# Optimization experiments

Measured on AMD Instinct MI355X. Metric: run time of the kernel, lower is better.

Reference implementation:

```python
import jax, jax.numpy as jnp
import numpy as np

B, S, D, H = 2, 2048, 1024, 16
DK = D // H


def setup_inputs() -> dict:
    key = jax.random.key(0)
    ks = jax.random.split(key, 11)
    scale = jnp.float32(1.0 / np.sqrt(D))
    inp = {
        "query": jax.random.normal(ks[0], (B, S, D), jnp.float32),
        "key": jax.random.normal(ks[1], (B, S, D), jnp.float32),
        "value": jax.random.normal(ks[2], (B, S, D), jnp.float32),
        # causal mask: True = masked (masked_fill semantics), broadcast over batch/heads
        "mask": jnp.triu(jnp.ones((S, S), dtype=bool), k=1)[None, None, :, :],
        "Wq": jax.random.normal(ks[3], (D, D), jnp.float32) * scale,
        "bq": jnp.zeros((D,), jnp.float32),
        "Wk": jax.random.normal(ks[4], (D, D), jnp.float32) * scale,
        "bk": jnp.zeros((D,), jnp.float32),
        "Wv": jax.random.normal(ks[5], (D, D), jnp.float32) * scale,
        "bv": jnp.zeros((D,), jnp.float32),
        "Wo": jax.random.normal(ks[6], (D, D), jnp.float32) * scale,
        "bo": jnp.zeros((D,), jnp.float32),
    }
    return inp


def _split_heads(x):
    # (B, S, D) -> (B, H, S, DK)
    b, s, _ = x.shape
    return x.reshape(b, s, H, DK).transpose(0, 2, 1, 3)


def reference(query, key, value, mask, Wq, bq, Wk, bk, Wv, bv, Wo, bo):
    # nn.Linear: y = x @ W.T + b
    q = _split_heads(query @ Wq.T + bq)
    k = _split_heads(key @ Wk.T + bk)
    v = _split_heads(value @ Wv.T + bv)

    inv_sqrt_dk = jnp.float32(1.0 / np.sqrt(DK))
    scores = jnp.einsum("bhqd,bhkd->bhqk", q, k) * inv_sqrt_dk  # (B,H,S,S)
    scores = jnp.where(mask, jnp.float32(-jnp.inf), scores)
    weights = jax.nn.softmax(scores, axis=-1)
    weights = jnp.nan_to_num(weights, nan=0.0)  # fully-masked rows -> 0

    attn = jnp.einsum("bhqk,bhkd->bhqd", weights, v)  # (B,H,S,DK)
    merged = attn.transpose(0, 2, 1, 3).reshape(B, S, D)  # merge heads
    return merged @ Wo.T + bo
```

## Files before the change

### kernel.cpp

```cpp
#include <hip/hip_runtime.h>


typedef unsigned short u16;
typedef unsigned int u32;
typedef __attribute__((ext_vector_type(8))) __bf16 bf16x8;
typedef __attribute__((ext_vector_type(8))) unsigned short us8;
typedef __attribute__((ext_vector_type(4))) float f32x4;

#define S_LEN 2048
#define D_DIM 1024
#define NH 16
#define DKH 64
#define Mi 1048576ULL

__device__ __forceinline__ u16 f2bf(float f) {
  return __builtin_bit_cast(u16, (__bf16)f);
}
__device__ __forceinline__ bf16x8 ld_frag(const u16* p) {
  us8 v = *(const us8*)p;
  return __builtin_bit_cast(bf16x8, v);
}
__device__ __forceinline__ void gl2lds16(const u16* g, u16* l) {
  __builtin_amdgcn_global_load_lds(
      (__attribute__((address_space(1))) void*)(g),
      (__attribute__((address_space(3))) void*)(l), 16, 0, 0);
}

__global__ __launch_bounds__(256, 1) void cvt_all(
    const float* __restrict__ q, const float* __restrict__ k, const float* __restrict__ v,
    const float* __restrict__ wq, const float* __restrict__ wk,
    const float* __restrict__ wv, const float* __restrict__ wo,
    u16* __restrict__ dst)
{
  size_t e0 = ((size_t)blockIdx.x * 256 + threadIdx.x) * 8;
  const float* s;
  if      (e0 <  4*Mi) s = q  + e0;
  else if (e0 <  8*Mi) s = k  + (e0 - 4*Mi);
  else if (e0 < 12*Mi) s = v  + (e0 - 8*Mi);
  else if (e0 < 13*Mi) s = wq + (e0 - 12*Mi);
  else if (e0 < 14*Mi) s = wk + (e0 - 13*Mi);
  else if (e0 < 15*Mi) s = wv + (e0 - 14*Mi);
  else                 s = wo + (e0 - 15*Mi);
  float4 a = ((const float4*)s)[0];
  float4 b = ((const float4*)s)[1];
  us8 o;
  o[0]=f2bf(a.x); o[1]=f2bf(a.y); o[2]=f2bf(a.z); o[3]=f2bf(a.w);
  o[4]=f2bf(b.x); o[5]=f2bf(b.y); o[6]=f2bf(b.z); o[7]=f2bf(b.w);
  *(us8*)(dst + e0) = o;
}

__global__ __launch_bounds__(256, 1) void gemm_qkv_bb(
    const u16* __restrict__ Aq, const u16* __restrict__ Ak, const u16* __restrict__ Av,
    const u16* __restrict__ Wqb, const u16* __restrict__ Wkb, const u16* __restrict__ Wvb,
    const float* __restrict__ bq, const float* __restrict__ bk, const float* __restrict__ bv,
    u16* __restrict__ Oq, u16* __restrict__ Ok, u16* __restrict__ Ov, float qscale)
{
  const int z = blockIdx.z;
  const u16* A = (z == 0) ? Aq : (z == 1) ? Ak : Av;
  const u16* W = (z == 0) ? Wqb : (z == 1) ? Wkb : Wvb;
  const float* bias = (z == 0) ? bq : (z == 1) ? bk : bv;
  u16* out = (z == 0) ? Oq : (z == 1) ? Ok : Ov;
  const float scale = (z == 0) ? qscale : 1.0f;
  const int K = 1024;

  __shared__ u16 lA[128 * 32];
  __shared__ u16 lB[128 * 32];
  const int t = threadIdx.x;
  const int w = t >> 6, l = t & 63;
  const int mblk = blockIdx.y * 128, nblk = blockIdx.x * 128;
  const int wm = (w & 1) * 64, wn = (w >> 1) * 64;
  const int lr = l & 15, lq = l >> 4;
  const int srow = l >> 2, scol = (l & 3) * 8;

  f32x4 acc[4][4] = {};

  for (int k0 = 0; k0 < K; k0 += 32) {
    __syncthreads();
    #pragma unroll
    for (int r = 0; r < 2; ++r) {
      int grp = r * 4 + w;
      gl2lds16(A + (size_t)(mblk + grp * 16 + srow) * K + k0 + scol, &lA[grp * 512]);
      gl2lds16(W + (size_t)(nblk + grp * 16 + srow) * K + k0 + scol, &lB[grp * 512]);
    }
    __syncthreads();
    bf16x8 aF[4], bF[4];
    #pragma unroll
    for (int mt = 0; mt < 4; ++mt)
      aF[mt] = ld_frag(&lA[(wm + mt * 16 + lr) * 32 + lq * 8]);
    #pragma unroll
    for (int nt = 0; nt < 4; ++nt)
      bF[nt] = ld_frag(&lB[(wn + nt * 16 + lr) * 32 + lq * 8]);
    #pragma unroll
    for (int mt = 0; mt < 4; ++mt)
      #pragma unroll
      for (int nt = 0; nt < 4; ++nt)
        acc[mt][nt] = __builtin_amdgcn_mfma_f32_16x16x32_bf16(aF[mt], bF[nt], acc[mt][nt], 0, 0, 0);
  }

  #pragma unroll
  for (int mt = 0; mt < 4; ++mt)
    #pragma unroll
    for (int nt = 0; nt < 4; ++nt)
      #pragma unroll
      for (int r = 0; r < 4; ++r) {
        int rowg = mblk + wm + mt * 16 + lq * 4 + r;
        int colg = nblk + wn + nt * 16 + lr;
        float v = (acc[mt][nt][r] + bias[colg]) * scale;
        int b = rowg >> 11, s = rowg & 2047;
        int h = colg >> 6, dk = colg & 63;
        if (z != 2)
          out[(((size_t)(b * NH + h)) * S_LEN + s) * DKH + dk] = f2bf(v);
        else
          out[(((size_t)(b * NH + h)) * DKH + dk) * S_LEN + s] = f2bf(v);
      }
}

__global__ __launch_bounds__(256, 1) void gemm_out_bb(
    const u16* __restrict__ A, const u16* __restrict__ W,
    const float* __restrict__ bias, float* __restrict__ out)
{
  const int K = 1024;
  __shared__ u16 lA[128 * 32];
  __shared__ u16 lB[64 * 32];
  const int t = threadIdx.x;
  const int w = t >> 6, l = t & 63;
  const int mblk = blockIdx.y * 128, nblk = blockIdx.x * 64;
  const int wm = (w & 1) * 64, wn = (w >> 1) * 32;
  const int lr = l & 15, lq = l >> 4;
  const int srow = l >> 2, scol = (l & 3) * 8;

  f32x4 acc[4][2] = {};

  for (int k0 = 0; k0 < K; k0 += 32) {
    __syncthreads();
    #pragma unroll
    for (int r = 0; r < 2; ++r) {
      int grp = r * 4 + w;
      gl2lds16(A + (size_t)(mblk + grp * 16 + srow) * K + k0 + scol, &lA[grp * 512]);
    }
    gl2lds16(W + (size_t)(nblk + w * 16 + srow) * K + k0 + scol, &lB[w * 512]);
    __syncthreads();
    bf16x8 aF[4], bF[2];
    #pragma unroll
    for (int mt = 0; mt < 4; ++mt)
      aF[mt] = ld_frag(&lA[(wm + mt * 16 + lr) * 32 + lq * 8]);
    #pragma unroll
    for (int nt = 0; nt < 2; ++nt)
      bF[nt] = ld_frag(&lB[(wn + nt * 16 + lr) * 32 + lq * 8]);
    #pragma unroll
    for (int mt = 0; mt < 4; ++mt)
      #pragma unroll
      for (int nt = 0; nt < 2; ++nt)
        acc[mt][nt] = __builtin_amdgcn_mfma_f32_16x16x32_bf16(aF[mt], bF[nt], acc[mt][nt], 0, 0, 0);
  }

  #pragma unroll
  for (int mt = 0; mt < 4; ++mt)
    #pragma unroll
    for (int nt = 0; nt < 2; ++nt)
      #pragma unroll
      for (int r = 0; r < 4; ++r) {
        int rowg = mblk + wm + mt * 16 + lq * 4 + r;
        int colg = nblk + wn + nt * 16 + lr;
        out[(size_t)rowg * D_DIM + colg] = acc[mt][nt][r] + bias[colg];
      }
}

__global__ __launch_bounds__(256, 1) void attn_fused(
    const u16* __restrict__ Q, const u16* __restrict__ K,
    const u16* __restrict__ Vt, u16* __restrict__ O)
{
  __shared__ u16 lK[2][64 * 64];
  __shared__ u16 lV[2][64 * 64];

  const int idx = blockIdx.x;
  const int s_ = idx >> 8;
  const int r_ = idx & 255;
  const int bh = r_ & 31;
  const int t_ = r_ >> 5;
  const int qt = (s_ == 0) ? t_ : (s_ == 1) ? 31 - t_ : (s_ == 2) ? 8 + t_ : 23 - t_;
  const int b = bh >> 4, h = bh & 15;
  const int t = threadIdx.x;
  const int w = t >> 6, l = t & 63;
  const int lr = l & 15, lq = l >> 4;

  const u16* Qp = Q + (size_t)bh * S_LEN * DKH;
  const u16* Kp = K + (size_t)bh * S_LEN * DKH;
  const u16* Vp = Vt + (size_t)bh * DKH * S_LEN;

  const int srow8 = l >> 3;
  const int schunk = l & 7;

  const int qrow = qt * 64 + w * 16 + lr;
  bf16x8 qf[2];
  qf[0] = ld_frag(Qp + (size_t)qrow * DKH + lq * 8);
  qf[1] = ld_frag(Qp + (size_t)qrow * DKH + 32 + lq * 8);

  f32x4 o[4] = {};
  f32x4 li4 = {};

  #pragma unroll
  for (int r2 = 0; r2 < 2; ++r2) {
    int grp = r2 * 4 + w;
    int row = grp * 8 + srow8;
    int sw = (row & 3) | (((row >> 3) & 1) << 2);
    int c = schunk ^ sw;
    gl2lds16(Kp + (size_t)row * DKH + c * 8, &lK[0][grp * 512]);
    gl2lds16(Vp + (size_t)row * S_LEN + c * 8, &lV[0][grp * 512]);
  }

  for (int kt = 0; kt <= qt; ++kt) {
    const int cur = kt & 1;
    __syncthreads();

    if (kt < qt) {
      #pragma unroll
      for (int r2 = 0; r2 < 2; ++r2) {
        int grp = r2 * 4 + w;
        int row = grp * 8 + srow8;
        int sw = (row & 3) | (((row >> 3) & 1) << 2);
        int c = schunk ^ sw;
        gl2lds16(Kp + (size_t)((kt + 1) * 64 + row) * DKH + c * 8, &lK[cur ^ 1][grp * 512]);
        gl2lds16(Vp + (size_t)row * S_LEN + (kt + 1) * 64 + c * 8, &lV[cur ^ 1][grp * 512]);
      }
    }

    f32x4 st[4] = {};
    #pragma unroll
    for (int ksd = 0; ksd < 2; ++ksd)
      #pragma unroll
      for (int nt = 0; nt < 4; ++nt) {
        int sig = 32 * (nt >> 1) + 8 * (lr >> 2) + 4 * (nt & 1) + (lr & 3);
        int slot = (ksd * 4 + lq) ^ (lr & 7);
        bf16x8 kb = ld_frag(&lK[cur][sig * 64 + slot * 8]);
        st[nt] = __builtin_amdgcn_mfma_f32_16x16x32_bf16(kb, qf[ksd], st[nt], 0, 0, 0);
      }

    float p[4][4];
    const bool diag = (kt == qt);
    const int qloc = w * 16 + lr;
    #pragma unroll
    for (int nt = 0; nt < 4; ++nt)
      #pragma unroll
      for (int r = 0; r < 4; ++r) {
        int kk = 32 * (nt >> 1) + 8 * lq + 4 * (nt & 1) + r;
        float e = exp2f(st[nt][r]);
        p[nt][r] = (diag && kk > qloc) ? 0.0f : e;
        li4[r] += p[nt][r];
      }

    #pragma unroll
    for (int ks = 0; ks < 2; ++ks) {
      us8 av;
      #pragma unroll
      for (int j = 0; j < 4; ++j) {
        av[j] = f2bf(p[2 * ks][j]);
        av[4 + j] = f2bf(p[2 * ks + 1][j]);
      }
      bf16x8 pa = __builtin_bit_cast(bf16x8, av);
      #pragma unroll
      for (int dblk = 0; dblk < 4; ++dblk) {
        int d = dblk * 16 + lr;
        int sw = (d & 3) | (((d >> 3) & 1) << 2);
        int slot = (4 * ks + lq) ^ sw;
        bf16x8 vb = ld_frag(&lV[cur][d * 64 + slot * 8]);
        o[dblk] = __builtin_amdgcn_mfma_f32_16x16x32_bf16(pa, vb, o[dblk], 0, 0, 0);
      }
    }
  }

  float li = li4[0] + li4[1] + li4[2] + li4[3];
  li += __shfl_xor(li, 16);
  li += __shfl_xor(li, 32);
  float ri[4];
  #pragma unroll
  for (int r = 0; r < 4; ++r) ri[r] = 1.0f / __shfl(li, lq * 4 + r);

  const size_t obase = ((size_t)b * S_LEN + qt * 64 + w * 16) * D_DIM + h * DKH;
  #pragma unroll
  for (int dblk = 0; dblk < 4; ++dblk)
    #pragma unroll
    for (int r = 0; r < 4; ++r)
      O[obase + (size_t)(lq * 4 + r) * D_DIM + dblk * 16 + lr] = f2bf(o[dblk][r] * ri[r]);
}

extern "C" void kernel_launch(void* const* d_in, const int* in_sizes, int n_in,
                              void* d_out, int out_size, void* d_ws, size_t ws_size,
                              hipStream_t stream) {
  const float* query = (const float*)d_in[0];
  const float* key   = (const float*)d_in[1];
  const float* value = (const float*)d_in[2];
  const float* Wq = (const float*)d_in[4];
  const float* bq = (const float*)d_in[5];
  const float* Wk = (const float*)d_in[6];
  const float* bk = (const float*)d_in[7];
  const float* Wv = (const float*)d_in[8];
  const float* bv = (const float*)d_in[9];
  const float* Wo = (const float*)d_in[10];
  const float* bo = (const float*)d_in[11];
  float* out = (float*)d_out;

  const float qscale = 0.125f * 1.44269504088896341f;
  dim3 blk(256);

  u16* base = (u16*)d_ws;
  u16* Qb = base;
  u16* Kb = base + 4 * Mi;
  u16* Vb = base + 8 * Mi;

  u16* cvt = base + 12 * Mi;
  u16* qbf = cvt;
  u16* kbf = cvt + 4 * Mi;
  u16* vbf = cvt + 8 * Mi;
  u16* wqb = cvt + 12 * Mi;
  u16* wkb = cvt + 13 * Mi;
  u16* wvb = cvt + 14 * Mi;
  u16* wob = cvt + 15 * Mi;
  u16* Ab  = qbf;

  cvt_all<<<dim3(8192), blk, 0, stream>>>(query, key, value, Wq, Wk, Wv, Wo, cvt);
  gemm_qkv_bb<<<dim3(8, 32, 3), blk, 0, stream>>>(qbf, kbf, vbf, wqb, wkb, wvb,
                                                  bq, bk, bv, Qb, Kb, Vb, qscale);
  attn_fused<<<dim3(1024), blk, 0, stream>>>(Qb, Kb, Vb, Ab);
  gemm_out_bb<<<dim3(16, 32), blk, 0, stream>>>(Ab, wob, bo, out);
}
```

Measured before the change: 233.4 us.

## Rewrite QKV projection GEMM as 256x256 8-wave ping-pong pipelined kernel

Replaces the 128x128 single-buffered QKV GEMM with a 256x256-tile, 512-thread kernel. It double-buffers LDS with global_load_lds prefetch, XOR-swizzles the LDS layout to avoid bank conflicts, interleaves the MFMA quadrants with fragment loads under s_setprio, and remaps block IDs across XCDs. The aim is to hide global-load latency and raise MFMA utilisation. In exchange it uses 128 KB of LDS and only 192 blocks, and the hand-placed waitcnt and barrier ordering is fragile.

Result: slower. 249.1 us (+6.7%).

```diff
diff --git a/kernel.cpp b/kernel.cpp
--- a/kernel.cpp
+++ b/kernel.cpp
@@ -49,63 +49,150 @@
   *(us8*)(dst + e0) = o;
 }
 
-__global__ __launch_bounds__(256, 1) void gemm_qkv_bb(
+__device__ __forceinline__ void stage_op(const u16* __restrict__ g, int rowbase, int k0,
+                                         u16* h0, u16* h1, int w, int srow, int scol) {
+  #pragma unroll
+  for (int hh = 0; hh < 2; ++hh) {
+    u16* dst = hh ? h1 : h0;
+    #pragma unroll
+    for (int i = 0; i < 2; ++i) {
+      int rr = hh * 128 + w * 16 + i * 8 + srow;
+      gl2lds16(g + (size_t)(rowbase + rr) * 1024 + k0 + scol, dst + (w * 2 + i) * 512);
+    }
+  }
+}
+
+__global__ __launch_bounds__(512, 2) void gemm_qkv_8p(
     const u16* __restrict__ Aq, const u16* __restrict__ Ak, const u16* __restrict__ Av,
     const u16* __restrict__ Wqb, const u16* __restrict__ Wkb, const u16* __restrict__ Wvb,
     const float* __restrict__ bq, const float* __restrict__ bk, const float* __restrict__ bv,
     u16* __restrict__ Oq, u16* __restrict__ Ok, u16* __restrict__ Ov, float qscale)
 {
-  const int z = blockIdx.z;
+  __shared__ u16 lds[2][4][8192];
+
+  const int o  = ((int)blockIdx.x & 7) * 24 + ((int)blockIdx.x >> 3);
+  const int z  = o >> 6;
+  const int r_ = o & 63;
+  const int mblk = (r_ >> 2) * 256;
+  const int nblk = (r_ & 3) * 256;
+
   const u16* A = (z == 0) ? Aq : (z == 1) ? Ak : Av;
   const u16* W = (z == 0) ? Wqb : (z == 1) ? Wkb : Wvb;
   const float* bias = (z == 0) ? bq : (z == 1) ? bk : bv;
   u16* out = (z == 0) ? Oq : (z == 1) ? Ok : Ov;
   const float scale = (z == 0) ? qscale : 1.0f;
-  const int K = 1024;
-
-  __shared__ u16 lA[128 * 32];
-  __shared__ u16 lB[128 * 32];
+
   const int t = threadIdx.x;
   const int w = t >> 6, l = t & 63;
-  const int mblk = blockIdx.y * 128, nblk = blockIdx.x * 128;
-  const int wm = (w & 1) * 64, wn = (w >> 1) * 64;
+  const int wr = w >> 2, wc = w & 3;
   const int lr = l & 15, lq = l >> 4;
-  const int srow = l >> 2, scol = (l & 3) * 8;
-
-  f32x4 acc[4][4] = {};
-
-  for (int k0 = 0; k0 < K; k0 += 32) {
-    __syncthreads();
-    #pragma unroll
-    for (int r = 0; r < 2; ++r) {
-      int grp = r * 4 + w;
-      gl2lds16(A + (size_t)(mblk + grp * 16 + srow) * K + k0 + scol, &lA[grp * 512]);
-      gl2lds16(W + (size_t)(nblk + grp * 16 + srow) * K + k0 + scol, &lB[grp * 512]);
-    }
-    __syncthreads();
-    bf16x8 aF[4], bF[4];
-    #pragma unroll
-    for (int mt = 0; mt < 4; ++mt)
-      aF[mt] = ld_frag(&lA[(wm + mt * 16 + lr) * 32 + lq * 8]);
+  const int srow = l >> 3;
+  const int scol = ((l & 7) ^ ((l >> 5) << 1)) * 8;
+  const int rb0 = (wc & 1) * 64;
+
+  #define IDX(r, kk) ((((r) * 64) + (kk) * 32 + lq * 8) ^ ((((r) >> 2) & 1) << 4))
+
+  f32x4 acc[8][4] = {};
+
+  stage_op(A, mblk, 0,  lds[0][0], lds[0][1], w, srow, scol);
+  stage_op(W, nblk, 0,  lds[0][2], lds[0][3], w, srow, scol);
+  stage_op(A, mblk, 64, lds[1][0], lds[1][1], w, srow, scol);
+  asm volatile("s_waitcnt vmcnt(4)" ::: "memory");
+  __builtin_amdgcn_s_barrier();
+
+  for (int kt = 0; kt < 16; ++kt) {
+    u16* lA = lds[kt & 1][wr];
+    u16* lB = lds[kt & 1][2 + (wc >> 1)];
+    u16 (*cur)[8192] = lds[kt & 1];
+    u16 (*nxt)[8192] = lds[(kt & 1) ^ 1];
+
+    bf16x8 aF[4][2], bF[4][2];
+
+    #pragma unroll
+    for (int am = 0; am < 4; ++am)
+      #pragma unroll
+      for (int kk = 0; kk < 2; ++kk)
+        aF[am][kk] = ld_frag(&lA[IDX(am * 16 + lr, kk)]);
+    #pragma unroll
+    for (int bn = 0; bn < 2; ++bn)
+      #pragma unroll
+      for (int kk = 0; kk < 2; ++kk)
+        bF[bn][kk] = ld_frag(&lB[IDX(rb0 + bn * 16 + lr, kk)]);
+    if (kt + 1 < 16) stage_op(W, nblk, (kt + 1) * 64, nxt[2], nxt[3], w, srow, scol);
+    __builtin_amdgcn_s_barrier();
+    asm volatile("s_waitcnt lgkmcnt(0)" ::: "memory");
+    __builtin_amdgcn_s_setprio(1);
+    #pragma unroll
+    for (int am = 0; am < 4; ++am)
+      #pragma unroll
+      for (int bn = 0; bn < 2; ++bn)
+        #pragma unroll
+        for (int kk = 0; kk < 2; ++kk)
+          acc[am][bn] = __builtin_amdgcn_mfma_f32_16x16x32_bf16(aF[am][kk], bF[bn][kk], acc[am][bn], 0, 0, 0);
+    __builtin_amdgcn_s_setprio(0);
+    __builtin_amdgcn_s_barrier();
+
+    #pragma unroll
+    for (int bn = 0; bn < 2; ++bn)
+      #pragma unroll
+      for (int kk = 0; kk < 2; ++kk)
+        bF[2 + bn][kk] = ld_frag(&lB[IDX(rb0 + 32 + bn * 16 + lr, kk)]);
+    __builtin_amdgcn_s_barrier();
+    asm volatile("s_waitcnt lgkmcnt(0)" ::: "memory");
+    __builtin_amdgcn_s_setprio(1);
+    #pragma unroll
+    for (int am = 0; am < 4; ++am)
+      #pragma unroll
+      for (int bn = 0; bn < 2; ++bn)
+        #pragma unroll
+        for (int kk = 0; kk < 2; ++kk)
+          acc[am][2 + bn] = __builtin_amdgcn_mfma_f32_16x16x32_bf16(aF[am][kk], bF[2 + bn][kk], acc[am][2 + bn], 0, 0, 0);
+    __builtin_amdgcn_s_setprio(0);
+    __builtin_amdgcn_s_barrier();
+
+    #pragma unroll
+    for (int am = 0; am < 4; ++am)
+      #pragma unroll
+      for (int kk = 0; kk < 2; ++kk)
+        aF[am][kk] = ld_frag(&lA[IDX(64 + am * 16 + lr, kk)]);
+    __builtin_amdgcn_s_barrier();
+    asm volatile("s_waitcnt lgkmcnt(0)" ::: "memory");
+    __builtin_amdgcn_s_setprio(1);
+    #pragma unroll
+    for (int am = 0; am < 4; ++am)
+      #pragma unroll
+      for (int bn = 0; bn < 2; ++bn)
+        #pragma unroll
+        for (int kk = 0; kk < 2; ++kk)
+          acc[4 + am][2 + bn] = __builtin_amdgcn_mfma_f32_16x16x32_bf16(aF[am][kk], bF[2 + bn][kk], acc[4 + am][2 + bn], 0, 0, 0);
+    __builtin_amdgcn_s_setprio(0);
+    __builtin_amdgcn_s_barrier();
+
+    if (kt + 2 < 16) stage_op(A, mblk, (kt + 2) * 64, cur[0], cur[1], w, srow, scol);
+    __builtin_amdgcn_s_setprio(1);
+    #pragma unroll
+    for (int am = 0; am < 4; ++am)
+      #pragma unroll
+      for (int bn = 0; bn < 2; ++bn)
+        #pragma unroll
+        for (int kk = 0; kk < 2; ++kk)
+          acc[4 + am][bn] = __builtin_amdgcn_mfma_f32_16x16x32_bf16(aF[am][kk], bF[bn][kk], acc[4 + am][bn], 0, 0, 0);
+    __builtin_amdgcn_s_setprio(0);
+    if (kt < 14)       asm volatile("s_waitcnt vmcnt(4)" ::: "memory");
+    else if (kt == 14) asm volatile("s_waitcnt vmcnt(0)" ::: "memory");
+    if (kt < 15) __builtin_amdgcn_s_barrier();
+  }
+  #undef IDX
+
+  #pragma unroll
+  for (int mt = 0; mt < 8; ++mt)
     #pragma unroll
     for (int nt = 0; nt < 4; ++nt)
-      bF[nt] = ld_frag(&lB[(wn + nt * 16 + lr) * 32 + lq * 8]);
-    #pragma unroll
-    for (int mt = 0; mt < 4; ++mt)
-      #pragma unroll
-      for (int nt = 0; nt < 4; ++nt)
-        acc[mt][nt] = __builtin_amdgcn_mfma_f32_16x16x32_bf16(aF[mt], bF[nt], acc[mt][nt], 0, 0, 0);
-  }
-
-  #pragma unroll
-  for (int mt = 0; mt < 4; ++mt)
-    #pragma unroll
-    for (int nt = 0; nt < 4; ++nt)
-      #pragma unroll
-      for (int r = 0; r < 4; ++r) {
-        int rowg = mblk + wm + mt * 16 + lq * 4 + r;
-        int colg = nblk + wn + nt * 16 + lr;
-        float v = (acc[mt][nt][r] + bias[colg]) * scale;
+      #pragma unroll
+      for (int rg = 0; rg < 4; ++rg) {
+        int rowg = mblk + wr * 128 + mt * 16 + lq * 4 + rg;
+        int colg = nblk + wc * 64 + nt * 16 + lr;
+        float v = (acc[mt][nt][rg] + bias[colg]) * scale;
         int b = rowg >> 11, s = rowg & 2047;
         int h = colg >> 6, dk = colg & 63;
         if (z != 2)
@@ -319,8 +406,8 @@
   u16* Ab  = qbf;
 
   cvt_all<<<dim3(8192), blk, 0, stream>>>(query, key, value, Wq, Wk, Wv, Wo, cvt);
-  gemm_qkv_bb<<<dim3(8, 32, 3), blk, 0, stream>>>(qbf, kbf, vbf, wqb, wkb, wvb,
-                                                  bq, bk, bv, Qb, Kb, Vb, qscale);
+  gemm_qkv_8p<<<dim3(192), dim3(512), 0, stream>>>(qbf, kbf, vbf, wqb, wkb, wvb,
+                                                   bq, bk, bv, Qb, Kb, Vb, qscale);
   attn_fused<<<dim3(1024), blk, 0, stream>>>(Qb, Kb, Vb, Ab);
   gemm_out_bb<<<dim3(16, 32), blk, 0, stream>>>(Ab, wob, bo, out);
 }
```

## Double-buffer LDS, swizzle LDS layout, and remap QKV GEMM blocks across XCDs

Applied to the files above, without the earlier changes.

Both bf16 GEMM kernels now use two LDS buffers. Each iteration prefetches the next K-slice while the current one feeds the MFMAs, which removes one barrier per iteration and overlaps global loads with compute. LDS columns are XOR-swizzled by row on both the store and the fragment-read side to reduce bank conflicts. The QKV GEMM moves to a 1D grid with a block-index remap that groups tiles per XCD for better L2 reuse. The cost is twice the shared memory and a dependence on async LDS loads completing at the single barrier.

After: 245.2 us. 5.1% more time.

```diff
diff --git a/kernel.cpp b/kernel.cpp
--- a/kernel.cpp
+++ b/kernel.cpp
@@ -55,7 +55,13 @@
     const float* __restrict__ bq, const float* __restrict__ bk, const float* __restrict__ bv,
     u16* __restrict__ Oq, u16* __restrict__ Ok, u16* __restrict__ Ov, float qscale)
 {
-  const int z = blockIdx.z;
+  const int bid = blockIdx.x;
+  const int o   = (bid & 7) * 96 + (bid >> 3);
+  const int z   = o >> 8;
+  const int rem = o & 255;
+  const int mblk = (rem >> 3) * 128;
+  const int nblk = (rem & 7) * 128;
+
   const u16* A = (z == 0) ? Aq : (z == 1) ? Ak : Av;
   const u16* W = (z == 0) ? Wqb : (z == 1) ? Wkb : Wvb;
   const float* bias = (z == 0) ? bq : (z == 1) ? bk : bv;
@@ -63,33 +69,43 @@
   const float scale = (z == 0) ? qscale : 1.0f;
   const int K = 1024;
 
-  __shared__ u16 lA[128 * 32];
-  __shared__ u16 lB[128 * 32];
+  __shared__ u16 lA[2][128 * 32];
+  __shared__ u16 lB[2][128 * 32];
   const int t = threadIdx.x;
   const int w = t >> 6, l = t & 63;
-  const int mblk = blockIdx.y * 128, nblk = blockIdx.x * 128;
   const int wm = (w & 1) * 64, wn = (w >> 1) * 64;
   const int lr = l & 15, lq = l >> 4;
-  const int srow = l >> 2, scol = (l & 3) * 8;
+  const int srow = l >> 2;
+  const int scol = ((l & 3) ^ ((l >> 3) & 3)) * 8;
+  const int rsw  = (lr >> 1) & 3;
 
   f32x4 acc[4][4] = {};
 
+  #pragma unroll
+  for (int r = 0; r < 2; ++r) {
+    int grp = r * 4 + w;
+    gl2lds16(A + (size_t)(mblk + grp * 16 + srow) * K + scol, &lA[0][grp * 512]);
+    gl2lds16(W + (size_t)(nblk + grp * 16 + srow) * K + scol, &lB[0][grp * 512]);
+  }
+
   for (int k0 = 0; k0 < K; k0 += 32) {
+    const int cur = (k0 >> 5) & 1;
     __syncthreads();
-    #pragma unroll
-    for (int r = 0; r < 2; ++r) {
-      int grp = r * 4 + w;
-      gl2lds16(A + (size_t)(mblk + grp * 16 + srow) * K + k0 + scol, &lA[grp * 512]);
-      gl2lds16(W + (size_t)(nblk + grp * 16 + srow) * K + k0 + scol, &lB[grp * 512]);
+    if (k0 + 32 < K) {
+      #pragma unroll
+      for (int r = 0; r < 2; ++r) {
+        int grp = r * 4 + w;
+        gl2lds16(A + (size_t)(mblk + grp * 16 + srow) * K + k0 + 32 + scol, &lA[cur ^ 1][grp * 512]);
+        gl2lds16(W + (size_t)(nblk + grp * 16 + srow) * K + k0 + 32 + scol, &lB[cur ^ 1][grp * 512]);
+      }
     }
-    __syncthreads();
     bf16x8 aF[4], bF[4];
     #pragma unroll
     for (int mt = 0; mt < 4; ++mt)
-      aF[mt] = ld_frag(&lA[(wm + mt * 16 + lr) * 32 + lq * 8]);
+      aF[mt] = ld_frag(&lA[cur][(wm + mt * 16 + lr) * 32 + (lq ^ rsw) * 8]);
     #pragma unroll
     for (int nt = 0; nt < 4; ++nt)
-      bF[nt] = ld_frag(&lB[(wn + nt * 16 + lr) * 32 + lq * 8]);
+      bF[nt] = ld_frag(&lB[cur][(wn + nt * 16 + lr) * 32 + (lq ^ rsw) * 8]);
     #pragma unroll
     for (int mt = 0; mt < 4; ++mt)
       #pragma unroll
@@ -120,33 +136,44 @@
     const float* __restrict__ bias, float* __restrict__ out)
 {
   const int K = 1024;
-  __shared__ u16 lA[128 * 32];
-  __shared__ u16 lB[64 * 32];
+  __shared__ u16 lA[2][128 * 32];
+  __shared__ u16 lB[2][64 * 32];
   const int t = threadIdx.x;
   const int w = t >> 6, l = t & 63;
   const int mblk = blockIdx.y * 128, nblk = blockIdx.x * 64;
   const int wm = (w & 1) * 64, wn = (w >> 1) * 32;
   const int lr = l & 15, lq = l >> 4;
-  const int srow = l >> 2, scol = (l & 3) * 8;
+  const int srow = l >> 2;
+  const int scol = ((l & 3) ^ ((l >> 3) & 3)) * 8;
+  const int rsw  = (lr >> 1) & 3;
 
   f32x4 acc[4][2] = {};
 
+  #pragma unroll
+  for (int r = 0; r < 2; ++r) {
+    int grp = r * 4 + w;
+    gl2lds16(A + (size_t)(mblk + grp * 16 + srow) * K + scol, &lA[0][grp * 512]);
+  }
+  gl2lds16(W + (size_t)(nblk + w * 16 + srow) * K + scol, &lB[0][w * 512]);
+
   for (int k0 = 0; k0 < K; k0 += 32) {
+    const int cur = (k0 >> 5) & 1;
     __syncthreads();
-    #pragma unroll
-    for (int r = 0; r < 2; ++r) {
-      int grp = r * 4 + w;
-      gl2lds16(A + (size_t)(mblk + grp * 16 + srow) * K + k0 + scol, &lA[grp * 512]);
+    if (k0 + 32 < K) {
+      #pragma unroll
+      for (int r = 0; r < 2; ++r) {
+        int grp = r * 4 + w;
+        gl2lds16(A + (size_t)(mblk + grp * 16 + srow) * K + k0 + 32 + scol, &lA[cur ^ 1][grp * 512]);
+      }
+      gl2lds16(W + (size_t)(nblk + w * 16 + srow) * K + k0 + 32 + scol, &lB[cur ^ 1][w * 512]);
     }
-    gl2lds16(W + (size_t)(nblk + w * 16 + srow) * K + k0 + scol, &lB[w * 512]);
-    __syncthreads();
     bf16x8 aF[4], bF[2];
     #pragma unroll
     for (int mt = 0; mt < 4; ++mt)
-      aF[mt] = ld_frag(&lA[(wm + mt * 16 + lr) * 32 + lq * 8]);
+      aF[mt] = ld_frag(&lA[cur][(wm + mt * 16 + lr) * 32 + (lq ^ rsw) * 8]);
     #pragma unroll
     for (int nt = 0; nt < 2; ++nt)
-      bF[nt] = ld_frag(&lB[(wn + nt * 16 + lr) * 32 + lq * 8]);
+      bF[nt] = ld_frag(&lB[cur][(wn + nt * 16 + lr) * 32 + (lq ^ rsw) * 8]);
     #pragma unroll
     for (int mt = 0; mt < 4; ++mt)
       #pragma unroll
@@ -319,8 +346,8 @@
   u16* Ab  = qbf;
 
   cvt_all<<<dim3(8192), blk, 0, stream>>>(query, key, value, Wq, Wk, Wv, Wo, cvt);
-  gemm_qkv_bb<<<dim3(8, 32, 3), blk, 0, stream>>>(qbf, kbf, vbf, wqb, wkb, wvb,
-                                                  bq, bk, bv, Qb, Kb, Vb, qscale);
+  gemm_qkv_bb<<<dim3(768), blk, 0, stream>>>(qbf, kbf, vbf, wqb, wkb, wvb,
+                                             bq, bk, bv, Qb, Kb, Vb, qscale);
   attn_fused<<<dim3(1024), blk, 0, stream>>>(Qb, Kb, Vb, Ab);
   gemm_out_bb<<<dim3(16, 32), blk, 0, stream>>>(Ab, wob, bo, out);
 }
```

## Double K-tile depth, XOR-swizzle LDS, and remap QKV GEMM block order

Applied to the files above, without the earlier changes.

Both projection GEMMs now stage 64-wide K tiles instead of 32, which halves the number of barrier-separated load phases. The LDS layout uses an XOR swizzle on 16-byte groups so fragment reads avoid bank conflicts. The QKV GEMM switches from a 3D grid to a 1D grid whose block index is remapped, likely to spread work across XCDs and improve L2 locality. In exchange, each block uses twice the LDS and there is still no double buffering.

New measurement: 242.9 us. +4.1%, slower.

```diff
diff --git a/kernel.cpp b/kernel.cpp
--- a/kernel.cpp
+++ b/kernel.cpp
@@ -55,7 +55,13 @@
     const float* __restrict__ bq, const float* __restrict__ bk, const float* __restrict__ bv,
     u16* __restrict__ Oq, u16* __restrict__ Ok, u16* __restrict__ Ov, float qscale)
 {
-  const int z = blockIdx.z;
+  const int bid = blockIdx.x;
+  const int o   = (bid & 7) * 96 + (bid >> 3);
+  const int z   = o >> 8;
+  const int rem = o & 255;
+  const int mblk = (rem >> 3) * 128;
+  const int nblk = (rem & 7) * 128;
+
   const u16* A = (z == 0) ? Aq : (z == 1) ? Ak : Av;
   const u16* W = (z == 0) ? Wqb : (z == 1) ? Wkb : Wvb;
   const float* bias = (z == 0) ? bq : (z == 1) ? bk : bv;
@@ -63,38 +69,42 @@
   const float scale = (z == 0) ? qscale : 1.0f;
   const int K = 1024;
 
-  __shared__ u16 lA[128 * 32];
-  __shared__ u16 lB[128 * 32];
+  __shared__ u16 lA[128 * 64];
+  __shared__ u16 lB[128 * 64];
   const int t = threadIdx.x;
   const int w = t >> 6, l = t & 63;
-  const int mblk = blockIdx.y * 128, nblk = blockIdx.x * 128;
   const int wm = (w & 1) * 64, wn = (w >> 1) * 64;
   const int lr = l & 15, lq = l >> 4;
-  const int srow = l >> 2, scol = (l & 3) * 8;
+  const int srow = l >> 3;
+  const int sgr  = (l & 7) ^ srow;
 
   f32x4 acc[4][4] = {};
 
-  for (int k0 = 0; k0 < K; k0 += 32) {
-    __syncthreads();
-    #pragma unroll
-    for (int r = 0; r < 2; ++r) {
-      int grp = r * 4 + w;
-      gl2lds16(A + (size_t)(mblk + grp * 16 + srow) * K + k0 + scol, &lA[grp * 512]);
-      gl2lds16(W + (size_t)(nblk + grp * 16 + srow) * K + k0 + scol, &lB[grp * 512]);
-    }
-    __syncthreads();
-    bf16x8 aF[4], bF[4];
-    #pragma unroll
-    for (int mt = 0; mt < 4; ++mt)
-      aF[mt] = ld_frag(&lA[(wm + mt * 16 + lr) * 32 + lq * 8]);
-    #pragma unroll
-    for (int nt = 0; nt < 4; ++nt)
-      bF[nt] = ld_frag(&lB[(wn + nt * 16 + lr) * 32 + lq * 8]);
-    #pragma unroll
-    for (int mt = 0; mt < 4; ++mt)
+  for (int k0 = 0; k0 < K; k0 += 64) {
+    __syncthreads();
+    #pragma unroll
+    for (int i = 0; i < 4; ++i) {
+      int chunk = w * 4 + i;
+      int row = chunk * 8 + srow;
+      gl2lds16(A + (size_t)(mblk + row) * K + k0 + sgr * 8, &lA[chunk * 512]);
+      gl2lds16(W + (size_t)(nblk + row) * K + k0 + sgr * 8, &lB[chunk * 512]);
+    }
+    __syncthreads();
+    #pragma unroll
+    for (int kk = 0; kk < 2; ++kk) {
+      bf16x8 aF[4], bF[4];
+      #pragma unroll
+      for (int mt = 0; mt < 4; ++mt)
+        aF[mt] = ld_frag(&lA[(wm + mt * 16 + lr) * 64 + ((kk * 4 + lq) ^ (lr & 7)) * 8]);
       #pragma unroll
       for (int nt = 0; nt < 4; ++nt)
-        acc[mt][nt] = __builtin_amdgcn_mfma_f32_16x16x32_bf16(aF[mt], bF[nt], acc[mt][nt], 0, 0, 0);
+        bF[nt] = ld_frag(&lB[(wn + nt * 16 + lr) * 64 + ((kk * 4 + lq) ^ (lr & 7)) * 8]);
+      #pragma unroll
+      for (int mt = 0; mt < 4; ++mt)
+        #pragma unroll
+        for (int nt = 0; nt < 4; ++nt)
+          acc[mt][nt] = __builtin_amdgcn_mfma_f32_16x16x32_bf16(aF[mt], bF[nt], acc[mt][nt], 0, 0, 0);
+    }
   }
 
   #pragma unroll
@@ -120,38 +130,48 @@
     const float* __restrict__ bias, float* __restrict__ out)
 {
   const int K = 1024;
-  __shared__ u16 lA[128 * 32];
-  __shared__ u16 lB[64 * 32];
+  __shared__ u16 lA[128 * 64];
+  __shared__ u16 lB[64 * 64];
   const int t = threadIdx.x;
   const int w = t >> 6, l = t & 63;
   const int mblk = blockIdx.y * 128, nblk = blockIdx.x * 64;
   const int wm = (w & 1) * 64, wn = (w >> 1) * 32;
   const int lr = l & 15, lq = l >> 4;
-  const int srow = l >> 2, scol = (l & 3) * 8;
+  const int srow = l >> 3;
+  const int sgr  = (l & 7) ^ srow;
 
   f32x4 acc[4][2] = {};
 
-  for (int k0 = 0; k0 < K; k0 += 32) {
-    __syncthreads();
-    #pragma unroll
-    for (int r = 0; r < 2; ++r) {
-      int grp = r * 4 + w;
-      gl2lds16(A + (size_t)(mblk + grp * 16 + srow) * K + k0 + scol, &lA[grp * 512]);
-    }
-    gl2lds16(W + (size_t)(nblk + w * 16 + srow) * K + k0 + scol, &lB[w * 512]);
-    __syncthreads();
-    bf16x8 aF[4], bF[2];
-    #pragma unroll
-    for (int mt = 0; mt < 4; ++mt)
-      aF[mt] = ld_frag(&lA[(wm + mt * 16 + lr) * 32 + lq * 8]);
-    #pragma unroll
-    for (int nt = 0; nt < 2; ++nt)
-      bF[nt] = ld_frag(&lB[(wn + nt * 16 + lr) * 32 + lq * 8]);
-    #pragma unroll
-    for (int mt = 0; mt < 4; ++mt)
+  for (int k0 = 0; k0 < K; k0 += 64) {
+    __syncthreads();
+    #pragma unroll
+    for (int i = 0; i < 4; ++i) {
+      int chunk = w * 4 + i;
+      int row = chunk * 8 + srow;
+      gl2lds16(A + (size_t)(mblk + row) * K + k0 + sgr * 8, &lA[chunk * 512]);
+    }
+    #pragma unroll
+    for (int i = 0; i < 2; ++i) {
+      int chunk = w * 2 + i;
+      int row = chunk * 8 + srow;
+      gl2lds16(W + (size_t)(nblk + row) * K + k0 + sgr * 8, &lB[chunk * 512]);
+    }
+    __syncthreads();
+    #pragma unroll
+    for (int kk = 0; kk < 2; ++kk) {
+      bf16x8 aF[4], bF[2];
+      #pragma unroll
+      for (int mt = 0; mt < 4; ++mt)
+        aF[mt] = ld_frag(&lA[(wm + mt * 16 + lr) * 64 + ((kk * 4 + lq) ^ (lr & 7)) * 8]);
       #pragma unroll
       for (int nt = 0; nt < 2; ++nt)
-        acc[mt][nt] = __builtin_amdgcn_mfma_f32_16x16x32_bf16(aF[mt], bF[nt], acc[mt][nt], 0, 0, 0);
+        bF[nt] = ld_frag(&lB[(wn + nt * 16 + lr) * 64 + ((kk * 4 + lq) ^ (lr & 7)) * 8]);
+      #pragma unroll
+      for (int mt = 0; mt < 4; ++mt)
+        #pragma unroll
+        for (int nt = 0; nt < 2; ++nt)
+          acc[mt][nt] = __builtin_amdgcn_mfma_f32_16x16x32_bf16(aF[mt], bF[nt], acc[mt][nt], 0, 0, 0);
+    }
   }
 
   #pragma unroll
@@ -319,8 +339,8 @@
   u16* Ab  = qbf;
 
   cvt_all<<<dim3(8192), blk, 0, stream>>>(query, key, value, Wq, Wk, Wv, Wo, cvt);
-  gemm_qkv_bb<<<dim3(8, 32, 3), blk, 0, stream>>>(qbf, kbf, vbf, wqb, wkb, wvb,
-                                                  bq, bk, bv, Qb, Kb, Vb, qscale);
+  gemm_qkv_bb<<<dim3(768), blk, 0, stream>>>(qbf, kbf, vbf, wqb, wkb, wvb,
+                                             bq, bk, bv, Qb, Kb, Vb, qscale);
   attn_fused<<<dim3(1024), blk, 0, stream>>>(Qb, Kb, Vb, Ab);
   gemm_out_bb<<<dim3(16, 32), blk, 0, stream>>>(Ab, wob, bo, out);
 }
```
